# Optimization experiments

Measured on AMD Instinct MI355X. Metric: run time of the kernel, lower is better.

## Reference

```python
import jax, jax.numpy as jnp
import numpy as np

BLOCK, HALO, HEADS = 8, 3, 4
WIN = BLOCK + 2 * HALO  # 14


def setup_inputs() -> dict:
    key = jax.random.key(0)
    k1, k2, k3, k4 = jax.random.split(key, 4)
    B, C, H, W = 4, 64, 192, 192
    d = C // HEADS
    return {
        "x": jax.random.normal(k1, (B, C, H, W), dtype=jnp.float32),
        "w_qkv": jax.random.normal(k2, (3 * C, C), dtype=jnp.float32) * 0.05,
        "rel_h": jax.random.normal(k3, (1, WIN, 1, d // 2), dtype=jnp.float32),
        "rel_w": jax.random.normal(k4, (1, 1, WIN, d // 2), dtype=jnp.float32),
    }


def _unfold_halo(t, nh, nw):
    B, C = t.shape[0], t.shape[1]
    tp = jnp.pad(t, ((0, 0), (0, 0), (HALO, HALO), (HALO, HALO)))
    ri = (jnp.arange(nh) * BLOCK)[:, None] + jnp.arange(WIN)
    ci = (jnp.arange(nw) * BLOCK)[:, None] + jnp.arange(WIN)
    p = tp[:, :, ri, :]
    p = p[:, :, :, :, ci]
    p = p.transpose(0, 2, 4, 3, 5, 1)
    return p.reshape(B * nh * nw, WIN * WIN, C)


def reference(x, w_qkv, rel_h, rel_w):
    B, C, H, W = x.shape
    d = C // HEADS
    nh, nw = H // BLOCK, W // BLOCK
    # 1x1 conv qkv
    qkv = jnp.einsum('bchw,oc->bohw', x, w_qkv)
    q, k, v = jnp.split(qkv, 3, axis=1)
    # q -> per-block tokens: (B*nh*nw, BLOCK*BLOCK, C)
    q = q.reshape(B, C, nh, BLOCK, nw, BLOCK).transpose(0, 2, 4, 3, 5, 1)
    q = q.reshape(B * nh * nw, BLOCK * BLOCK, C) * (d ** -0.5)
    k = _unfold_halo(k, nh, nw)
    v = _unfold_halo(v, nh, nw)
    # split heads: '(b) a (h d) -> (b h) a d'
    q = q.reshape(-1, BLOCK * BLOCK, HEADS, d).transpose(0, 2, 1, 3).reshape(-1, BLOCK * BLOCK, d)
    v = v.reshape(-1, WIN * WIN, HEADS, d).transpose(0, 2, 1, 3).reshape(-1, WIN * WIN, d)
    k = k.reshape(-1, WIN, WIN, HEADS, d).transpose(0, 3, 1, 2, 4).reshape(-1, WIN, WIN, d)
    # inline relative position bias added to keys
    kh, kw = k[..., : d // 2], k[..., d // 2:]
    k = jnp.concatenate([kh + rel_h, kw + rel_w], axis=-1).reshape(-1, WIN * WIN, d)
    sim = jnp.einsum('bid,bjd->bij', q, k)          # (BLh, 64, 196)
    attn = jax.nn.softmax(sim, axis=-1)
    out = jnp.einsum('bij,bjd->bid', attn, v)       # (BLh, 64, d)
    # fold back: '(b h w n) (k1 k2) d -> b (n d) (h k1) (w k2)'
    out = out.reshape(B, nh, nw, HEADS, BLOCK, BLOCK, d)
    out = out.transpose(0, 3, 6, 1, 4, 2, 5).reshape(B, HEADS * d, nh * BLOCK, nw * BLOCK)
    return out
```

## Files before the change

kernel.cpp:

```cpp
#include <hip/hip_runtime.h>
#include <hip/hip_bf16.h>

constexpr int B = 4, C = 64, H = 192, W = 192;
constexpr int HEADS = 4, D = 16;
constexpr int BLK = 8, HALO = 3, WIN = 14;
constexpr int NH = H / BLK, NW = W / BLK;
constexpr int HW = H * W;
constexpr int O = 3 * C;

constexpr int K_OFF = 0;
constexpr int VPLANE = 208 * 16 + 16;
constexpr int V_OFF = 208 * 64;
constexpr int RH_OFF = V_OFF + 4 * VPLANE;
constexpr int RW_OFF = RH_OFF + 128;
constexpr int LDS_TOT = RW_OFF + 128;

typedef __attribute__((ext_vector_type(4))) short short4v;
typedef __attribute__((ext_vector_type(8))) short short8v;
typedef __attribute__((ext_vector_type(8))) __bf16 bf16x8;
typedef __attribute__((ext_vector_type(4))) float f32x4;

__device__ inline f32x4 mfma_bf16(short8v a, short8v b, f32x4 c) {
  return __builtin_amdgcn_mfma_f32_16x16x32_bf16(
      __builtin_bit_cast(bf16x8, a), __builtin_bit_cast(bf16x8, b), c, 0, 0, 0);
}

__device__ inline unsigned short f2bf(float f) {
  __bf16 h = (__bf16)f;
  return __builtin_bit_cast(unsigned short, h);
}

__global__ __launch_bounds__(256) void qkv_mfma(
    const float* __restrict__ x, const float* __restrict__ w,
    unsigned short* __restrict__ qkv) {
  __shared__ unsigned short wlds[192 * 64];
  const int tid = threadIdx.x;

  const float4* wf4 = reinterpret_cast<const float4*>(w);
#pragma unroll
  for (int it = 0; it < 12; ++it) {
    const int idx = it * 256 + tid;
    const int o = idx >> 4;
    const int c = (idx & 15) << 2;
    const float4 wv = wf4[idx];
    ushort4 st;
    st.x = f2bf(wv.x);
    st.y = f2bf(wv.y);
    st.z = f2bf(wv.z);
    st.w = f2bf(wv.w);
    const int sw = (((c >> 3) ^ (o & 7)) << 3) + (c & 4);
    *reinterpret_cast<ushort4*>(&wlds[o * 64 + sw]) = st;
  }

  const int wave = tid >> 6, lane = tid & 63;
  const int p = lane & 15, g = lane >> 4;
  const int pix_w = blockIdx.x * 128 + wave * 32;
  const int b = pix_w / HW;
  const int hw = pix_w - b * HW + p;
  const float* xb = x + (size_t)b * C * HW;

  short8v xf[2][2];
#pragma unroll
  for (int pt = 0; pt < 2; ++pt) {
#pragma unroll
    for (int ks = 0; ks < 2; ++ks) {
      unsigned short u[8];
#pragma unroll
      for (int j = 0; j < 8; ++j)
        u[j] = f2bf(xb[(size_t)(ks * 32 + g * 8 + j) * HW + hw + pt * 16]);
      unsigned int pw[4];
#pragma unroll
      for (int e = 0; e < 4; ++e)
        pw[e] = (unsigned int)u[2 * e] | ((unsigned int)u[2 * e + 1] << 16);
      xf[pt][ks] = __builtin_bit_cast(short8v, *reinterpret_cast<uint4*>(pw));
    }
  }
  __syncthreads();

#pragma unroll
  for (int ot = 0; ot < 12; ++ot) {
    short8v af[2];
#pragma unroll
    for (int ks = 0; ks < 2; ++ks)
      af[ks] = *reinterpret_cast<const short8v*>(
          wlds + (ot * 16 + p) * 64 + (((((ks << 2) | g)) ^ (p & 7)) << 3));
    const float s = (ot < 4) ? 0.25f * 1.44269504f : 1.0f;
#pragma unroll
    for (int pt = 0; pt < 2; ++pt) {
      f32x4 acc = {0.f, 0.f, 0.f, 0.f};
      acc = mfma_bf16(af[0], xf[pt][0], acc);
      acc = mfma_bf16(af[1], xf[pt][1], acc);
      ushort4 st;
      st.x = f2bf(acc[0] * s);
      st.y = f2bf(acc[1] * s);
      st.z = f2bf(acc[2] * s);
      st.w = f2bf(acc[3] * s);
      *reinterpret_cast<ushort4*>(
          qkv + (size_t)(pix_w + pt * 16 + p) * O + ot * 16 + g * 4) = st;
    }
  }
}

__global__ __launch_bounds__(512, 4) void attn_kernel(
    const unsigned short* __restrict__ qkv,
    const float* __restrict__ rel_h, const float* __restrict__ rel_w,
    float* __restrict__ out) {
  __shared__ __align__(16) unsigned short lds[LDS_TOT];

  const int tid = threadIdx.x;
  const int blk = blockIdx.x;
  const int win = (blk & 7) * 288 + (blk >> 3);
  const int b = win / (NH * NW);
  const int wrem = win - b * (NH * NW);
  const int bh = wrem / NW;
  const int bw = wrem - bh * NW;
  const int y0 = bh * BLK - HALO;
  const int x0 = bw * BLK - HALO;

  if (tid < 256) {
    const int i = tid & 127;
    const int rr = i >> 3, cc = i & 7;
    const int rc = (rr < WIN) ? rr : (WIN - 1);
    const float* src = (tid < 128) ? rel_h : rel_w;
    lds[((tid < 128) ? RH_OFF : RW_OFF) + i] = f2bf(src[rc * 8 + cc]);
  }

  uint4 raw[7];
#pragma unroll
  for (int it = 0; it < 7; ++it) {
    const int item = tid + it * 512;
    const bool isK = item < 1664;
    const int li = isK ? item : item - 1664;
    const int pixel = li >> 3;
    const int g = li & 7;
    const int wy = pixel / WIN;
    const int wx = pixel - wy * WIN;
    const int y = y0 + wy, xx = x0 + wx;
    const bool inb =
        (item < 3328) & (y >= 0) & (y < H) & (xx >= 0) & (xx < W);
    uint4 rv = make_uint4(0u, 0u, 0u, 0u);
    if (inb)
      rv = *reinterpret_cast<const uint4*>(
          qkv + ((size_t)(b * HW + y * W + xx)) * O + (isK ? C : 2 * C) + g * 8);
    raw[it] = rv;
  }

  const int lane = tid & 63;
  const int wv = tid >> 6;
  const int head = wv & 3;
  const int qhalf = wv >> 2;
  const int r = lane & 15, hq = lane >> 4;
  short8v qf[2];
#pragma unroll
  for (int q2 = 0; q2 < 2; ++q2) {
    const int qrow = (qhalf * 2 + q2) * 16 + r;
    const int y = bh * BLK + (qrow >> 3);
    const int xx = bw * BLK + (qrow & 7);
    qf[q2] = *reinterpret_cast<const short8v*>(
        qkv + ((size_t)(b * HW + y * W + xx)) * O + head * D + (hq & 1) * 8);
  }

#pragma unroll
  for (int it = 0; it < 7; ++it) {
    const int item = tid + it * 512;
    if (item < 3328) {
      const bool isK = item < 1664;
      const int li = isK ? item : item - 1664;
      const int pixel = li >> 3;
      const int g = li & 7;
      if (isK) {
        const int ch = (g ^ pixel) & 7;
        *reinterpret_cast<uint4*>(&lds[K_OFF + pixel * 64 + ch * 8]) = raw[it];
      } else {
        const int hd = g >> 1, c8 = g & 1;
        *reinterpret_cast<uint4*>(
            &lds[V_OFF + hd * VPLANE + pixel * 16 + c8 * 8]) = raw[it];
      }
    }
  }
  __syncthreads();

  int koff[13];
#pragma unroll
  for (int t = 0; t < 13; ++t) {
    const int row = 16 * t + r;
    const int wy = row / WIN;
    const int wx = row - wy * WIN;
    const int a_k =
        K_OFF + row * 64 + ((((head << 1) | (hq & 1)) ^ (row & 7)) << 3);
    const int a_rh = RH_OFF + wy * 8;
    const int a_rw = RW_OFF + wx * 8;
    koff[t] = (hq < 2) ? a_k : ((hq == 2) ? a_rh : a_rw);
  }

  const unsigned vbase_addr =
      (unsigned)(unsigned long long)(const void*)&lds[V_OFF + head * VPLANE] +
      (unsigned)(lane * 8);
  short4v vlo[7], vhi[7];
#pragma unroll
  for (int tau = 0; tau < 7; ++tau) {
    const unsigned va = vbase_addr + tau * 1024;
    asm volatile("ds_read_b64_tr_b16 %0, %1" : "=v"(vlo[tau]) : "v"(va));
    if (tau < 6) {
      asm volatile("ds_read_b64_tr_b16 %0, %1 offset:512"
                   : "=v"(vhi[tau])
                   : "v"(va));
    } else {
      vhi[tau] = (short4v){0, 0, 0, 0};
    }
  }
  asm volatile("s_waitcnt lgkmcnt(0)" ::: "memory");
  __builtin_amdgcn_sched_barrier(0);

  __builtin_amdgcn_s_setprio(1);
  for (int q2 = 0; q2 < 2; ++q2) {
    f32x4 sim[13];
#pragma unroll
    for (int t = 0; t < 13; ++t) {
      const short8v kf = *reinterpret_cast<const short8v*>(&lds[koff[t]]);
      f32x4 z4 = {0.f, 0.f, 0.f, 0.f};
      sim[t] = mfma_bf16(kf, qf[q2], z4);
    }

    float sum = 0.f;
#pragma unroll
    for (int t = 0; t < 13; ++t) {
#pragma unroll
      for (int e = 0; e < 4; ++e) {
        float p = exp2f(sim[t][e]);
        if (t == 12 && hq >= 1) p = 0.f;
        sim[t][e] = p;
        sum += p;
      }
    }
    sum += __shfl_xor(sum, 16);
    sum += __shfl_xor(sum, 32);
    const float inv = 1.f / sum;

    f32x4 oacc = {0.f, 0.f, 0.f, 0.f};
#pragma unroll
    for (int tau = 0; tau < 7; ++tau) {
      short8v pf;
#pragma unroll
      for (int e = 0; e < 4; ++e) pf[e] = (short)f2bf(sim[2 * tau][e]);
#pragma unroll
      for (int e = 0; e < 4; ++e)
        pf[4 + e] =
            (2 * tau + 1 < 13) ? (short)f2bf(sim[2 * tau + 1][e]) : (short)0;
      const short8v vf = __builtin_shufflevector(vlo[tau], vhi[tau], 0, 1, 2,
                                                 3, 4, 5, 6, 7);
      oacc = mfma_bf16(vf, pf, oacc);
    }

    const int qrow = (qhalf * 2 + q2) * 16 + r;
    const int y = bh * BLK + (qrow >> 3);
    const int xx = bw * BLK + (qrow & 7);
    float* op = out + ((size_t)b * C + head * D + 4 * hq) * HW + y * W + xx;
#pragma unroll
    for (int e = 0; e < 4; ++e) op[(size_t)e * HW] = oacc[e] * inv;
  }
  __builtin_amdgcn_s_setprio(0);
}

extern "C" void kernel_launch(void* const* d_in, const int* in_sizes, int n_in,
                              void* d_out, int out_size, void* d_ws,
                              size_t ws_size, hipStream_t stream) {
  const float* x = (const float*)d_in[0];
  const float* w_qkv = (const float*)d_in[1];
  const float* rel_h = (const float*)d_in[2];
  const float* rel_w = (const float*)d_in[3];
  float* out = (float*)d_out;

  unsigned short* qkv = (unsigned short*)d_ws;

  qkv_mfma<<<B * HW / 128, 256, 0, stream>>>(x, w_qkv, qkv);
  attn_kernel<<<B * NH * NW, 512, 0, stream>>>(qkv, rel_h, rel_w, out);
}
```

Before: 76.88 us.

## Interleave QK, softmax and PV per key tile for both query tiles in attention

Restructures the attention inner loop so each key tile's QK MFMAs for both query sub-tiles are followed immediately by exp2 and the PV MFMA, instead of running two sequential passes over 13 score tiles. Each K fragment is read from LDS once and shared by both query tiles, and the full sim[13] array no longer has to stay live, which lowers register pressure and gives more independent MFMA chains to interleave. It also uses the raw exp2 intrinsic and packed bf16 conversion, and simplifies the bounds check to unsigned compares. Softmax normalization is still deferred to the end, so the maths is unchanged.

```diff
diff --git a/kernel.cpp b/kernel.cpp
--- a/kernel.cpp
+++ b/kernel.cpp
@@ -28,6 +28,12 @@
 __device__ inline unsigned short f2bf(float f) {
   __bf16 h = (__bf16)f;
   return __builtin_bit_cast(unsigned short, h);
+}
+
+__device__ inline unsigned cvt_pk_bf16(float a, float b) {
+  unsigned r;
+  asm("v_cvt_pk_bf16_f32 %0, %1, %2" : "=v"(r) : "v"(a), "v"(b));
+  return r;
 }
 
 __global__ __launch_bounds__(256) void qkv_mfma(
@@ -136,8 +142,8 @@
     const int wy = pixel / WIN;
     const int wx = pixel - wy * WIN;
     const int y = y0 + wy, xx = x0 + wx;
-    const bool inb =
-        (item < 3328) & (y >= 0) & (y < H) & (xx >= 0) & (xx < W);
+    const bool inb = (item < 3328) & ((unsigned)y < (unsigned)H) &
+                     ((unsigned)xx < (unsigned)W);
     uint4 rv = make_uint4(0u, 0u, 0u, 0u);
     if (inb)
       rv = *reinterpret_cast<const uint4*>(
@@ -150,14 +156,18 @@
   const int head = wv & 3;
   const int qhalf = wv >> 2;
   const int r = lane & 15, hq = lane >> 4;
-  short8v qf[2];
-#pragma unroll
-  for (int q2 = 0; q2 < 2; ++q2) {
-    const int qrow = (qhalf * 2 + q2) * 16 + r;
-    const int y = bh * BLK + (qrow >> 3);
-    const int xx = bw * BLK + (qrow & 7);
-    qf[q2] = *reinterpret_cast<const short8v*>(
+  const int qrow0 = qhalf * 32 + r;
+  short8v qf0, qf1;
+  {
+    const int y = bh * BLK + (qrow0 >> 3);
+    const int xx = bw * BLK + (qrow0 & 7);
+    qf0 = *reinterpret_cast<const short8v*>(
         qkv + ((size_t)(b * HW + y * W + xx)) * O + head * D + (hq & 1) * 8);
+    const int qrow1 = qrow0 + 16;
+    const int y1 = bh * BLK + (qrow1 >> 3);
+    const int xx1 = bw * BLK + (qrow1 & 7);
+    qf1 = *reinterpret_cast<const short8v*>(
+        qkv + ((size_t)(b * HW + y1 * W + xx1)) * O + head * D + (hq & 1) * 8);
   }
 
 #pragma unroll
@@ -213,51 +223,74 @@
   __builtin_amdgcn_sched_barrier(0);
 
   __builtin_amdgcn_s_setprio(1);
-  for (int q2 = 0; q2 < 2; ++q2) {
-    f32x4 sim[13];
-#pragma unroll
-    for (int t = 0; t < 13; ++t) {
-      const short8v kf = *reinterpret_cast<const short8v*>(&lds[koff[t]]);
-      f32x4 z4 = {0.f, 0.f, 0.f, 0.f};
-      sim[t] = mfma_bf16(kf, qf[q2], z4);
-    }
-
-    float sum = 0.f;
-#pragma unroll
-    for (int t = 0; t < 13; ++t) {
-#pragma unroll
-      for (int e = 0; e < 4; ++e) {
-        float p = exp2f(sim[t][e]);
-        if (t == 12 && hq >= 1) p = 0.f;
-        sim[t][e] = p;
-        sum += p;
+
+  f32x4 oacc0 = {0.f, 0.f, 0.f, 0.f}, oacc1 = {0.f, 0.f, 0.f, 0.f};
+  float sum0 = 0.f, sum1 = 0.f;
+#pragma unroll
+  for (int tau = 0; tau < 7; ++tau) {
+    unsigned pw0[4], pw1[4];
+#pragma unroll
+    for (int half = 0; half < 2; ++half) {
+      const int t = 2 * tau + half;
+      if (t < 13) {
+        const short8v kf = *reinterpret_cast<const short8v*>(&lds[koff[t]]);
+        const f32x4 z4 = {0.f, 0.f, 0.f, 0.f};
+        const f32x4 s0 = mfma_bf16(kf, qf0, z4);
+        const f32x4 s1 = mfma_bf16(kf, qf1, z4);
+        float p0e[4], p1e[4];
+#pragma unroll
+        for (int e = 0; e < 4; ++e) {
+          float pa = __builtin_amdgcn_exp2f(s0[e]);
+          float pb = __builtin_amdgcn_exp2f(s1[e]);
+          if (t == 12 && hq >= 1) {
+            pa = 0.f;
+            pb = 0.f;
+          }
+          sum0 += pa;
+          sum1 += pb;
+          p0e[e] = pa;
+          p1e[e] = pb;
+        }
+        pw0[half * 2 + 0] = cvt_pk_bf16(p0e[0], p0e[1]);
+        pw0[half * 2 + 1] = cvt_pk_bf16(p0e[2], p0e[3]);
+        pw1[half * 2 + 0] = cvt_pk_bf16(p1e[0], p1e[1]);
+        pw1[half * 2 + 1] = cvt_pk_bf16(p1e[2], p1e[3]);
+      } else {
+        pw0[2] = 0u;
+        pw0[3] = 0u;
+        pw1[2] = 0u;
+        pw1[3] = 0u;
       }
     }
-    sum += __shfl_xor(sum, 16);
-    sum += __shfl_xor(sum, 32);
-    const float inv = 1.f / sum;
-
-    f32x4 oacc = {0.f, 0.f, 0.f, 0.f};
-#pragma unroll
-    for (int tau = 0; tau < 7; ++tau) {
-      short8v pf;
-#pragma unroll
-      for (int e = 0; e < 4; ++e) pf[e] = (short)f2bf(sim[2 * tau][e]);
-#pragma unroll
-      for (int e = 0; e < 4; ++e)
-        pf[4 + e] =
-            (2 * tau + 1 < 13) ? (short)f2bf(sim[2 * tau + 1][e]) : (short)0;
-      const short8v vf = __builtin_shufflevector(vlo[tau], vhi[tau], 0, 1, 2,
-                                                 3, 4, 5, 6, 7);
-      oacc = mfma_bf16(vf, pf, oacc);
-    }
-
-    const int qrow = (qhalf * 2 + q2) * 16 + r;
-    const int y = bh * BLK + (qrow >> 3);
-    const int xx = bw * BLK + (qrow & 7);
+    const short8v vf =
+        __builtin_shufflevector(vlo[tau], vhi[tau], 0, 1, 2, 3, 4, 5, 6, 7);
+    const uint4 u0 = make_uint4(pw0[0], pw0[1], pw0[2], pw0[3]);
+    const uint4 u1 = make_uint4(pw1[0], pw1[1], pw1[2], pw1[3]);
+    oacc0 = mfma_bf16(vf, __builtin_bit_cast(short8v, u0), oacc0);
+    oacc1 = mfma_bf16(vf, __builtin_bit_cast(short8v, u1), oacc1);
+  }
+
+  sum0 += __shfl_xor(sum0, 16);
+  sum0 += __shfl_xor(sum0, 32);
+  sum1 += __shfl_xor(sum1, 16);
+  sum1 += __shfl_xor(sum1, 32);
+  const float inv0 = 1.f / sum0;
+  const float inv1 = 1.f / sum1;
+
+  {
+    const int y = bh * BLK + (qrow0 >> 3);
+    const int xx = bw * BLK + (qrow0 & 7);
     float* op = out + ((size_t)b * C + head * D + 4 * hq) * HW + y * W + xx;
 #pragma unroll
-    for (int e = 0; e < 4; ++e) op[(size_t)e * HW] = oacc[e] * inv;
+    for (int e = 0; e < 4; ++e) op[(size_t)e * HW] = oacc0[e] * inv0;
+  }
+  {
+    const int qrow1 = qrow0 + 16;
+    const int y = bh * BLK + (qrow1 >> 3);
+    const int xx = bw * BLK + (qrow1 & 7);
+    float* op = out + ((size_t)b * C + head * D + 4 * hq) * HW + y * W + xx;
+#pragma unroll
+    for (int e = 0; e < 4; ++e) op[(size_t)e * HW] = oacc1[e] * inv1;
   }
   __builtin_amdgcn_s_setprio(0);
 }
```

Result: faster. 63.29 us (-17.7%).
